# Kernel tuning notes

Measured on AMD Instinct MI355X. Metric: run time of the kernel, lower is better.

## Reference

```python
import jax, jax.numpy as jnp
import numpy as np
import math

BS, C, H, W, D = 2, 64, 32, 16, 32
FLAT = H * W * D          # 16384 voxels
N = 2048                  # non-empty voxels per sample (fixed for jit)
K = 256                   # min(int(0.2 * N), max_k=256)
EPS = 1e-5


def _pe(c, length):
    # sinusoidal positional encoding, interleaved sin/cos as in the torch code
    pos = jnp.arange(length, dtype=jnp.float32)[:, None]
    div = jnp.exp(jnp.arange(0, c, 2, dtype=jnp.float32) * (-math.log(10000.0) / c))
    ang = pos * div[None, :]                     # [length, c//2]
    return jnp.stack([jnp.sin(ang), jnp.cos(ang)], axis=-1).reshape(length, c)


def _bn(z, g, b):
    # eval-mode BatchNorm1d with running_mean=0, running_var=1
    return z * (g / jnp.sqrt(1.0 + EPS)) + b


def setup_inputs() -> dict:
    key = jax.random.key(0)
    ks = jax.random.split(key, 8)
    rng = np.random.default_rng(0)
    mask_idx = np.stack([np.sort(rng.choice(FLAT, size=N, replace=False)) for _ in range(BS)])
    w = lambda k, s: jax.random.normal(k, s, jnp.float32) * 0.05
    return dict(
        input=jax.random.normal(ks[0], (BS, C, H, W, D), jnp.float32),
        mask_idx=jnp.asarray(mask_idx, jnp.int32),
        w_ne1=w(ks[1], (C, 32)), b_ne1=jnp.zeros(32), g_ne=jnp.ones(32), be_ne=jnp.zeros(32),
        w_ne2=w(ks[2], (32, 1)), b_ne2=jnp.zeros(1),
        w_p1=w(ks[3], (C, 32)), b_p1=jnp.zeros(32), g_p1=jnp.ones(32), be_p1=jnp.zeros(32),
        w_p2=w(ks[4], (32, 32)), b_p2=jnp.zeros(32), g_p2=jnp.ones(32), be_p2=jnp.zeros(32),
        w_p3=w(ks[5], (32, 1)), b_p3=jnp.zeros(1),
        w_r1=w(ks[6], (4 * C, 2 * C)), b_r1=jnp.zeros(2 * C),
        w_r2=w(ks[7], (2 * C, C)), b_r2=jnp.zeros(C),
    )


def reference(input, mask_idx, w_ne1, b_ne1, g_ne, be_ne, w_ne2, b_ne2,
              w_p1, b_p1, g_p1, be_p1, w_p2, b_p2, g_p2, be_p2, w_p3, b_p3,
              w_r1, b_r1, w_r2, b_r2):
    bs, c = input.shape[0], input.shape[1]
    pe = _pe(c, FLAT)
    x = input                         # agg (external Bottleneck3D stack) ~ identity
    x_flat = x.reshape(bs, c, FLAT)

    def per_sample(xf, idx, key):
        mpe = pe[idx]                                  # [N, c] masked positional enc
        xi = xf[:, idx].T + mpe                        # [N, c] masked gather
        h1 = jax.nn.relu(_bn(xi @ w_ne1 + b_ne1, g_ne, be_ne))
        prob = jax.nn.sigmoid((h1 @ w_ne2 + b_ne2)[:, 0])    # [N] non-empty prob
        # torch.multinomial(prob, K, replacement=True)
        topk = jax.random.categorical(key, jnp.log(prob), shape=(K,))
        tf = xi[topk]                                  # [K, c] sampled features
        ne_k = prob[topk]                              # [K]
        # xi_repeat + tiled masked_pe[topk]  ->  [N, K, c]
        xw = xi[:, None, :] + mpe[topk][None, :, :]
        hp = jax.nn.relu(_bn(xw @ w_p1 + b_p1, g_p1, be_p1))
        hp = jax.nn.relu(_bn(hp @ w_p2 + b_p2, g_p2, be_p2))
        P = jax.nn.sigmoid((hp @ w_p3 + b_p3)[..., 0])  # [N, K]
        Pi = P * ne_k[None, :]
        Pe_ = (1.0 - P) * ne_k[None, :]
        x_intra = (Pi @ tf) / jnp.sum(Pi, axis=1, keepdims=True)   # [N, c]
        x_inter = (Pe_ @ tf) / jnp.sum(Pe_, axis=1, keepdims=True)
        ctx = jnp.zeros((2 * c, FLAT), input.dtype)
        ctx = ctx.at[:c, idx].set(x_intra.T).at[c:, idx].set(x_inter.T)
        return ctx

    keys = jax.random.split(jax.random.key(42), bs)
    ctx = jax.vmap(per_sample)(x_flat, mask_idx, keys).reshape(bs, 2 * c, H, W, D)
    xcat = jnp.concatenate([input, ctx, x], axis=1)     # [bs, 4c, H, W, D]
    # resize: the two defined 1x1 Conv3d layers (Bottleneck3D blocks are external)
    y = jnp.einsum('bchwd,cf->bfhwd', xcat, w_r1) + b_r1[None, :, None, None, None]
    y = jnp.einsum('bchwd,cf->bfhwd', y, w_r2) + b_r2[None, :, None, None, None]
    return y
```

## Files before the change

### kernel.cpp

```cpp
#include <hip/hip_runtime.h>
#include <cstdint>
#include <cmath>

#define BS    2
#define CC    64
#define FLAT  16384
#define NN    2048
#define KK    256
#define EPSBN 1e-5f
#define TINYF 1.17549435e-38f
#define PE_SCALE -0.14391156831212787f
#define JAX_PARTITIONABLE 1

#define OFF_XI    0
#define OFF_XI1   (OFF_XI   + BS*NN*CC)
#define OFF_PROB  (OFF_XI1  + BS*NN*32)
#define OFF_LOGP  (OFF_PROB + BS*NN)
#define OFF_NEK   (OFF_LOGP + BS*NN)
#define OFF_TF    (OFF_NEK  + BS*KK)
#define OFF_M1    (OFF_TF   + BS*KK*CC)
#define OFF_DELTA (OFF_M1   + BS*KK*32)
#define OFF_WF    (OFF_DELTA+ BS*NN*CC)
#define OFF_BF    (OFF_WF   + 256*CC)
#define OFF_INV   (OFF_BF   + CC)

__device__ __forceinline__ uint32_t rotl32(uint32_t x, int r) {
  return (x << r) | (x >> (32 - r));
}
__device__ __forceinline__ void tf2x32(uint32_t k0, uint32_t k1,
                                       uint32_t& x0, uint32_t& x1) {
  uint32_t k2 = k0 ^ k1 ^ 0x1BD11BDAu;
  x0 += k0; x1 += k1;
#define TFR(r) { x0 += x1; x1 = rotl32(x1, r); x1 ^= x0; }
  TFR(13) TFR(15) TFR(26) TFR(6)  x0 += k1; x1 += k2 + 1u;
  TFR(17) TFR(29) TFR(16) TFR(24) x0 += k2; x1 += k0 + 2u;
  TFR(13) TFR(15) TFR(26) TFR(6)  x0 += k0; x1 += k1 + 3u;
  TFR(17) TFR(29) TFR(16) TFR(24) x0 += k1; x1 += k2 + 4u;
  TFR(13) TFR(15) TFR(26) TFR(6)  x0 += k2; x1 += k0 + 5u;
#undef TFR
}
__device__ __forceinline__ void jax_key(int b, uint32_t& k0, uint32_t& k1) {
#if JAX_PARTITIONABLE
  uint32_t x0 = 0u, x1 = (uint32_t)b;
  tf2x32(0u, 42u, x0, x1);
  k0 = x0; k1 = x1;
#else
  uint32_t a0 = 0u, a1 = 2u, c0 = 1u, c1 = 3u;
  tf2x32(0u, 42u, a0, a1);
  tf2x32(0u, 42u, c0, c1);
  if (b == 0) { k0 = a0; k1 = c0; } else { k0 = a1; k1 = c1; }
#endif
}
__device__ __forceinline__ uint32_t jax_bits(uint32_t k0, uint32_t k1, uint32_t i) {
#if JAX_PARTITIONABLE
  uint32_t x0 = 0u, x1 = i;
  tf2x32(k0, k1, x0, x1);
  return x0 ^ x1;
#else
  const uint32_t half = (uint32_t)(KK * NN) / 2u;
  uint32_t x0, x1;
  if (i < half) { x0 = i; x1 = i + half; tf2x32(k0, k1, x0, x1); return x0; }
  else          { x0 = i - half; x1 = i; tf2x32(k0, k1, x0, x1); return x1; }
#endif
}

__global__ void k0_fold(const float* __restrict__ w_r1, const float* __restrict__ b_r1,
                        const float* __restrict__ w_r2, const float* __restrict__ b_r2,
                        float* __restrict__ ws) {
  int c = blockIdx.x;
  int co = threadIdx.x;
  float acc = 0.f;
  for (int f = 0; f < 128; ++f)
    acc += w_r1[c * 128 + f] * w_r2[f * 64 + co];
  ws[OFF_WF + c * 64 + co] = acc;
  if (blockIdx.x == 0) {
    float bb = b_r2[co];
    for (int f = 0; f < 128; ++f) bb += b_r1[f] * w_r2[f * 64 + co];
    ws[OFF_BF + co] = bb;
  }
  int* inv = (int*)(ws + OFF_INV);
  int t = blockIdx.x * 64 + threadIdx.x;
  inv[t] = -1;
  inv[t + BS * FLAT / 2] = -1;
}

__global__ __launch_bounds__(256) void k1_xi(
    const float* __restrict__ input, const int* __restrict__ midx,
    const float* __restrict__ w_ne1, const float* __restrict__ b_ne1,
    const float* __restrict__ g_ne,  const float* __restrict__ be_ne,
    const float* __restrict__ w_ne2, const float* __restrict__ b_ne2,
    const float* __restrict__ w_p1,  const float* __restrict__ g_p1,
    float* __restrict__ ws) {
  int tid = threadIdx.x;
  int j = tid & 31, nl = tid >> 5;
  int bn = blockIdx.x * 8 + nl;
  int b = bn >> 11, n = bn & (NN - 1);
  int pos = midx[b * NN + n];
  __shared__ float xis[8][66];
  float d = expf((float)(2 * j) * PE_SCALE);
  float ang = (float)pos * d;
  float xs = sinf(ang) + input[((size_t)(b * CC + 2 * j)) * FLAT + pos];
  float xc = cosf(ang) + input[((size_t)(b * CC + 2 * j + 1)) * FLAT + pos];
  xis[nl][2 * j] = xs; xis[nl][2 * j + 1] = xc;
  float2 v2; v2.x = xs; v2.y = xc;
  ((float2*)(ws + OFF_XI + (size_t)(b * NN + n) * CC))[j] = v2;
  __syncthreads();
  float zne = b_ne1[j];
  float z1 = 0.f;
#pragma unroll
  for (int c2 = 0; c2 < CC; ++c2) {
    float xv = xis[nl][c2];
    zne += xv * w_ne1[c2 * 32 + j];
    z1  += xv * w_p1[c2 * 32 + j];
  }
  float ane = g_ne[j] / sqrtf(1.f + EPSBN);
  float h = fmaxf(0.f, zne * ane + be_ne[j]);
  float pp = h * w_ne2[j];
  for (int off = 16; off > 0; off >>= 1) pp += __shfl_down(pp, off, 32);
  if (j == 0) {
    float prob = 1.f / (1.f + expf(-(pp + b_ne2[0])));
    ws[OFF_PROB + b * NN + n] = prob;
    ws[OFF_LOGP + b * NN + n] = logf(prob);
    ((int*)(ws + OFF_INV))[b * FLAT + pos] = n;
  }
  float a1 = g_p1[j] / sqrtf(1.f + EPSBN);
  ws[OFF_XI1 + (size_t)(b * NN + n) * 32 + j] = z1 * a1;
}

__global__ __launch_bounds__(256) void k2_sample(
    const int* __restrict__ midx,
    const float* __restrict__ w_p1, const float* __restrict__ b_p1,
    const float* __restrict__ g_p1, const float* __restrict__ be_p1,
    float* __restrict__ ws) {
  int b = blockIdx.x >> 8, k = blockIdx.x & 255;
  int tid = threadIdx.x;
  uint32_t kb0, kb1;
  jax_key(b, kb0, kb1);
  const float* logp = ws + OFF_LOGP + b * NN;
  const float NEGINF = -__builtin_inff();
  float bv = NEGINF; int bn = NN;
#pragma unroll 1
  for (int r = 0; r < 8; ++r) {
    int n = r * 256 + tid;
    uint32_t bits = jax_bits(kb0, kb1, (uint32_t)(k * NN + n));
    float f = __uint_as_float(0x3f800000u | (bits >> 9)) - 1.0f;
    float u = fmaxf(TINYF, f + TINYF);
    float gmb = -logf(-logf(u));
    float v = logp[n] + gmb;
    if (v > bv || (v == bv && n < bn)) { bv = v; bn = n; }
  }
  __shared__ float sv[256];
  __shared__ int   sn[256];
  __shared__ float mpe[CC];
  sv[tid] = bv; sn[tid] = bn;
  __syncthreads();
  for (int s = 128; s > 0; s >>= 1) {
    if (tid < s) {
      float v2 = sv[tid + s]; int n2 = sn[tid + s];
      if (v2 > sv[tid] || (v2 == sv[tid] && n2 < sn[tid])) { sv[tid] = v2; sn[tid] = n2; }
    }
    __syncthreads();
  }
  int best = sn[0];
  if (tid == 0)
    ws[OFF_NEK + b * KK + k] = ws[OFF_PROB + b * NN + best];
  if (tid < CC) {
    int c = tid;
    ws[OFF_TF + (size_t)(b * KK + k) * CC + c] =
        ws[OFF_XI + (size_t)(b * NN + best) * CC + c];
    int pos = midx[b * NN + best];
    int jj = c >> 1;
    float ang = (float)pos * expf((float)(2 * jj) * PE_SCALE);
    mpe[c] = (c & 1) ? cosf(ang) : sinf(ang);
  }
  __syncthreads();
  if (tid < 32) {
    int jj = tid;
    float acc = b_p1[jj];
#pragma unroll
    for (int c = 0; c < CC; ++c) acc += mpe[c] * w_p1[c * 32 + jj];
    float a = g_p1[jj] / sqrtf(1.f + EPSBN);
    ws[OFF_M1 + (size_t)(b * KK + k) * 32 + jj] = acc * a + be_p1[jj];
  }
}

__global__ __launch_bounds__(256) void k3_fused(
    const float* __restrict__ w_p2, const float* __restrict__ b_p2,
    const float* __restrict__ g_p2, const float* __restrict__ be_p2,
    const float* __restrict__ w_p3, const float* __restrict__ b_p3,
    float* __restrict__ ws) {
  __shared__ __align__(16) float m1t[32 * 132];
  __shared__ __align__(16) float w2s[1024];
  __shared__ __align__(16) float Pis[4][256];
  __shared__ __align__(16) float nekl[256];
  __shared__ __align__(16) float xi1s[4][32];
  __shared__ __align__(16) float c2f[32];
  __shared__ __align__(16) float w3l[32];
  __shared__ float sI[4], sE[4];
  int tid = threadIdx.x;
  int b = blockIdx.x >> 9;
  int n0 = (blockIdx.x & 511) * 4;
  int nn  = tid >> 6;
  int kgl = (tid >> 2) & 15;
  int qg  = tid & 3;
  int k0l = kgl * 8, q0 = qg * 8;
  for (int e = tid; e < 1024; e += 256) {
    int q = e & 31;
    w2s[e] = w_p2[e] * (g_p2[q] / sqrtf(1.f + EPSBN));
  }
  if (tid < 32) {
    c2f[tid] = b_p2[tid] * (g_p2[tid] / sqrtf(1.f + EPSBN)) + be_p2[tid];
    w3l[tid] = w_p3[tid];
  }
  if (tid < 128) {
    int n4 = tid >> 5, jx = tid & 31;
    xi1s[n4][jx] = ws[OFF_XI1 + (size_t)(b * NN + n0 + n4) * 32 + jx];
  }
  nekl[tid] = ws[OFF_NEK + b * KK + tid];
  float b3 = b_p3[0];
  __syncthreads();
  float4 cva = *(const float4*)&c2f[q0];
  float4 cvb = *(const float4*)&c2f[q0 + 4];
  float4 w3a = *(const float4*)&w3l[q0];
  float4 w3b = *(const float4*)&w3l[q0 + 4];
#pragma unroll 1
  for (int kh = 0; kh < 2; ++kh) {
    for (int e = tid; e < 1024; e += 256) {
      int kl = e >> 3, q = e & 7;
      float4 v = *(const float4*)(ws + OFF_M1 +
                   (size_t)(b * KK + kh * 128 + kl) * 32 + q * 4);
      m1t[(q * 4 + 0) * 132 + kl] = v.x;
      m1t[(q * 4 + 1) * 132 + kl] = v.y;
      m1t[(q * 4 + 2) * 132 + kl] = v.z;
      m1t[(q * 4 + 3) * 132 + kl] = v.w;
    }
    __syncthreads();
    float z[8][8];
#pragma unroll
    for (int i = 0; i < 8; ++i) {
      z[i][0] = cva.x; z[i][1] = cva.y; z[i][2] = cva.z; z[i][3] = cva.w;
      z[i][4] = cvb.x; z[i][5] = cvb.y; z[i][6] = cvb.z; z[i][7] = cvb.w;
    }
#pragma unroll 4
    for (int jj = 0; jj < 32; ++jj) {
      float xv = xi1s[nn][jj];
      const float4* mr = (const float4*)&m1t[jj * 132 + k0l];
      float4 ma = mr[0], mb = mr[1];
      const float4* wr = (const float4*)&w2s[jj * 32 + q0];
      float4 wa = wr[0], wb = wr[1];
      float h0 = fmaxf(0.f, xv + ma.x), h1 = fmaxf(0.f, xv + ma.y);
      float h2 = fmaxf(0.f, xv + ma.z), h3 = fmaxf(0.f, xv + ma.w);
      float h4 = fmaxf(0.f, xv + mb.x), h5 = fmaxf(0.f, xv + mb.y);
      float h6 = fmaxf(0.f, xv + mb.z), h7 = fmaxf(0.f, xv + mb.w);
#define ZROW(i, hh) \
      z[i][0] += hh * wa.x; z[i][1] += hh * wa.y; z[i][2] += hh * wa.z; z[i][3] += hh * wa.w; \
      z[i][4] += hh * wb.x; z[i][5] += hh * wb.y; z[i][6] += hh * wb.z; z[i][7] += hh * wb.w;
      ZROW(0, h0) ZROW(1, h1) ZROW(2, h2) ZROW(3, h3)
      ZROW(4, h4) ZROW(5, h5) ZROW(6, h6) ZROW(7, h7)
#undef ZROW
    }
    float s[8];
#pragma unroll
    for (int i = 0; i < 8; ++i)
      s[i] = fmaxf(0.f, z[i][0]) * w3a.x + fmaxf(0.f, z[i][1]) * w3a.y
           + fmaxf(0.f, z[i][2]) * w3a.z + fmaxf(0.f, z[i][3]) * w3a.w
           + fmaxf(0.f, z[i][4]) * w3b.x + fmaxf(0.f, z[i][5]) * w3b.y
           + fmaxf(0.f, z[i][6]) * w3b.z + fmaxf(0.f, z[i][7]) * w3b.w;
#pragma unroll
    for (int i = 0; i < 8; ++i) {
      s[i] += __shfl_xor(s[i], 1, 64);
      s[i] += __shfl_xor(s[i], 2, 64);
    }
    float sv0 = qg < 2 ? (qg == 0 ? s[0] : s[1]) : (qg == 2 ? s[2] : s[3]);
    float sv1 = qg < 2 ? (qg == 0 ? s[4] : s[5]) : (qg == 2 ? s[6] : s[7]);
    int kg0 = kh * 128 + k0l;
    float P0 = 1.f / (1.f + expf(-(sv0 + b3)));
    float P1 = 1.f / (1.f + expf(-(sv1 + b3)));
    Pis[nn][kg0 + qg]     = P0 * nekl[kg0 + qg];
    Pis[nn][kg0 + 4 + qg] = P1 * nekl[kg0 + 4 + qg];
    __syncthreads();
  }
  float* xIl = m1t;
  float* xEl = m1t + 272;
  if (tid < 128) {
    int n4 = tid >> 5, jx = tid & 31;
    float s1 = 0.f, s2 = 0.f;
#pragma unroll
    for (int t = 0; t < 8; ++t) {
      float pi = Pis[n4][jx + 32 * t];
      s1 += pi;
      s2 += nekl[jx + 32 * t] - pi;
    }
    for (int off = 16; off > 0; off >>= 1) {
      s1 += __shfl_down(s1, off, 32);
      s2 += __shfl_down(s2, off, 32);
    }
    if (jx == 0) { sI[n4] = s1; sE[n4] = s2; }
  }
  __syncthreads();
  {
    int c = tid & 63, n = tid >> 6;
    const float4* PI4 = (const float4*)Pis[n];
    const float4* NE4 = (const float4*)nekl;
    const float* tfg = ws + OFF_TF + (size_t)b * KK * CC + c;
    float aI = 0.f, aE = 0.f;
#pragma unroll 4
    for (int kq = 0; kq < 64; ++kq) {
      float4 piv = PI4[kq], nev = NE4[kq];
      float t0 = tfg[(4 * kq + 0) * 64];
      float t1 = tfg[(4 * kq + 1) * 64];
      float t2 = tfg[(4 * kq + 2) * 64];
      float t3 = tfg[(4 * kq + 3) * 64];
      aI += piv.x * t0 + piv.y * t1 + piv.z * t2 + piv.w * t3;
      aE += (nev.x - piv.x) * t0 + (nev.y - piv.y) * t1
          + (nev.z - piv.z) * t2 + (nev.w - piv.w) * t3;
    }
    xIl[n * 68 + c] = aI / sI[n];
    xEl[n * 68 + c] = aE / sE[n];
  }
  __syncthreads();
  {
    int co = tid & 63, n4 = tid >> 6;
    const float4* xI4 = (const float4*)&xIl[n4 * 68];
    const float4* xE4 = (const float4*)&xEl[n4 * 68];
    const float* wI = ws + OFF_WF + 64 * CC + co;
    const float* wE = ws + OFF_WF + 128 * CC + co;
    float dsum = 0.f;
#pragma unroll 4
    for (int cq = 0; cq < 16; ++cq) {
      float4 xi4 = xI4[cq], xe4 = xE4[cq];
      dsum += xi4.x * wI[(4 * cq + 0) * 64] + xi4.y * wI[(4 * cq + 1) * 64]
            + xi4.z * wI[(4 * cq + 2) * 64] + xi4.w * wI[(4 * cq + 3) * 64];
      dsum += xe4.x * wE[(4 * cq + 0) * 64] + xe4.y * wE[(4 * cq + 1) * 64]
            + xe4.z * wE[(4 * cq + 2) * 64] + xe4.w * wE[(4 * cq + 3) * 64];
    }
    ws[OFF_DELTA + (size_t)(b * NN + n0 + n4) * CC + co] = dsum;
  }
}

__global__ __launch_bounds__(256) void k4_out(
    const float* __restrict__ input, float* __restrict__ out,
    const float* __restrict__ ws) {
  __shared__ __align__(16) float wfa[64 * 64];
  __shared__ float bfl[64];
  int tid = threadIdx.x;
  const float* wf = ws + OFF_WF;
  for (int e = tid; e < 4096; e += 256) {
    int c = e >> 6, co = e & 63;
    wfa[e] = wf[c * 64 + co] + wf[(192 + c) * 64 + co];
  }
  if (tid < 64) bfl[tid] = ws[OFF_BF + tid];
  __syncthreads();
  int q = tid >> 6, lane = tid & 63;
  int pg = blockIdx.x * 64 + lane;
  int b = pg >> 14, pos = pg & (FLAT - 1);
  const int* inv = (const int*)(ws + OFF_INV);
  float acc[16];
#pragma unroll
  for (int u = 0; u < 16; ++u) acc[u] = bfl[q * 16 + u];
#pragma unroll 4
  for (int c = 0; c < 64; ++c) {
    float xv = input[((size_t)(b * CC + c)) * FLAT + pos];
    const float4* wr = (const float4*)&wfa[c * 64 + q * 16];
#pragma unroll
    for (int u4 = 0; u4 < 4; ++u4) {
      float4 w = wr[u4];
      acc[u4 * 4 + 0] += xv * w.x; acc[u4 * 4 + 1] += xv * w.y;
      acc[u4 * 4 + 2] += xv * w.z; acc[u4 * 4 + 3] += xv * w.w;
    }
  }
  int n = inv[pg];
  if (n >= 0) {
    const float4* dr = (const float4*)(ws + OFF_DELTA + (size_t)(b * NN + n) * CC + q * 16);
#pragma unroll
    for (int u4 = 0; u4 < 4; ++u4) {
      float4 dv = dr[u4];
      acc[u4 * 4 + 0] += dv.x; acc[u4 * 4 + 1] += dv.y;
      acc[u4 * 4 + 2] += dv.z; acc[u4 * 4 + 3] += dv.w;
    }
  }
#pragma unroll
  for (int u = 0; u < 16; ++u)
    out[((size_t)(b * CC + q * 16 + u)) * FLAT + pos] = acc[u];
}

extern "C" void kernel_launch(void* const* d_in, const int* in_sizes, int n_in,
                              void* d_out, int out_size, void* d_ws, size_t ws_size,
                              hipStream_t stream) {
  const float* input = (const float*)d_in[0];
  const int*   midx  = (const int*)  d_in[1];
  const float* w_ne1 = (const float*)d_in[2];
  const float* b_ne1 = (const float*)d_in[3];
  const float* g_ne  = (const float*)d_in[4];
  const float* be_ne = (const float*)d_in[5];
  const float* w_ne2 = (const float*)d_in[6];
  const float* b_ne2 = (const float*)d_in[7];
  const float* w_p1  = (const float*)d_in[8];
  const float* b_p1  = (const float*)d_in[9];
  const float* g_p1  = (const float*)d_in[10];
  const float* be_p1 = (const float*)d_in[11];
  const float* w_p2  = (const float*)d_in[12];
  const float* b_p2  = (const float*)d_in[13];
  const float* g_p2  = (const float*)d_in[14];
  const float* be_p2 = (const float*)d_in[15];
  const float* w_p3  = (const float*)d_in[16];
  const float* b_p3  = (const float*)d_in[17];
  const float* w_r1  = (const float*)d_in[18];
  const float* b_r1  = (const float*)d_in[19];
  const float* w_r2  = (const float*)d_in[20];
  const float* b_r2  = (const float*)d_in[21];
  float* out = (float*)d_out;
  float* ws  = (float*)d_ws;

  k0_fold<<<dim3(256), dim3(64), 0, stream>>>(w_r1, b_r1, w_r2, b_r2, ws);
  k1_xi<<<dim3(BS * NN / 8), dim3(256), 0, stream>>>(
      input, midx, w_ne1, b_ne1, g_ne, be_ne, w_ne2, b_ne2, w_p1, g_p1, ws);
  k2_sample<<<dim3(BS * KK), dim3(256), 0, stream>>>(
      midx, w_p1, b_p1, g_p1, be_p1, ws);
  k3_fused<<<dim3(BS * NN / 4), dim3(256), 0, stream>>>(
      w_p2, b_p2, g_p2, be_p2, w_p3, b_p3, ws);
  k4_out<<<dim3(BS * FLAT / 64), dim3(256), 0, stream>>>(input, out, ws);
}
```

Measured before the change: 182.1 us.

## Shrink per-thread register tiles in k3 and split k4 output channels across blocks

In k3, each thread now accumulates an 8x4 tile instead of 8x8 and loops over two k-halves, and the M1 transpose load uses unpadded rows with a different thread mapping. xIl/xEl get their own shared arrays instead of aliasing m1t. In k4, each block now computes only 16 of the 64 output channels, giving four times as many blocks with smaller weight tiles and fewer accumulators. The aim is lower register pressure and higher occupancy, at the cost of re-reading the input four times in k4 and possible LDS bank conflicts from removing the padding.

```diff
diff --git a/kernel.cpp b/kernel.cpp
--- a/kernel.cpp
+++ b/kernel.cpp
@@ -189,21 +189,22 @@
     const float* __restrict__ g_p2, const float* __restrict__ be_p2,
     const float* __restrict__ w_p3, const float* __restrict__ b_p3,
     float* __restrict__ ws) {
-  __shared__ __align__(16) float m1t[32 * 132];
+  __shared__ __align__(16) float m1t[32 * 128];
   __shared__ __align__(16) float w2s[1024];
   __shared__ __align__(16) float Pis[4][256];
   __shared__ __align__(16) float nekl[256];
   __shared__ __align__(16) float xi1s[4][32];
   __shared__ __align__(16) float c2f[32];
   __shared__ __align__(16) float w3l[32];
+  __shared__ __align__(16) float xIl[4 * 68], xEl[4 * 68];
   __shared__ float sI[4], sE[4];
   int tid = threadIdx.x;
   int b = blockIdx.x >> 9;
   int n0 = (blockIdx.x & 511) * 4;
-  int nn  = tid >> 6;
-  int kgl = (tid >> 2) & 15;
-  int qg  = tid & 3;
-  int k0l = kgl * 8, q0 = qg * 8;
+  int nn = tid >> 6;
+  int kg = (tid >> 3) & 7;
+  int qg = tid & 7;
+  int q0 = qg * 4;
   for (int e = tid; e < 1024; e += 256) {
     int q = e & 31;
     w2s[e] = w_p2[e] * (g_p2[q] / sqrtf(1.f + EPSBN));
@@ -219,69 +220,69 @@
   nekl[tid] = ws[OFF_NEK + b * KK + tid];
   float b3 = b_p3[0];
   __syncthreads();
-  float4 cva = *(const float4*)&c2f[q0];
-  float4 cvb = *(const float4*)&c2f[q0 + 4];
-  float4 w3a = *(const float4*)&w3l[q0];
-  float4 w3b = *(const float4*)&w3l[q0 + 4];
+  const float4* w2s4 = (const float4*)w2s;
+  const float4 cv  = *(const float4*)&c2f[q0];
+  const float4 w3v = *(const float4*)&w3l[q0];
 #pragma unroll 1
   for (int kh = 0; kh < 2; ++kh) {
-    for (int e = tid; e < 1024; e += 256) {
-      int kl = e >> 3, q = e & 7;
-      float4 v = *(const float4*)(ws + OFF_M1 +
-                   (size_t)(b * KK + kh * 128 + kl) * 32 + q * 4);
-      m1t[(q * 4 + 0) * 132 + kl] = v.x;
-      m1t[(q * 4 + 1) * 132 + kl] = v.y;
-      m1t[(q * 4 + 2) * 132 + kl] = v.z;
-      m1t[(q * 4 + 3) * 132 + kl] = v.w;
+    {
+      int kl = tid & 127, jh = tid >> 7;
+      const float4* src = (const float4*)(ws + OFF_M1 +
+                           (size_t)(b * KK + kh * 128 + kl) * 32 + jh * 16);
+#pragma unroll
+      for (int u = 0; u < 4; ++u) {
+        float4 v = src[u];
+        m1t[(jh * 16 + u * 4 + 0) * 128 + kl] = v.x;
+        m1t[(jh * 16 + u * 4 + 1) * 128 + kl] = v.y;
+        m1t[(jh * 16 + u * 4 + 2) * 128 + kl] = v.z;
+        m1t[(jh * 16 + u * 4 + 3) * 128 + kl] = v.w;
+      }
     }
     __syncthreads();
-    float z[8][8];
-#pragma unroll
-    for (int i = 0; i < 8; ++i) {
-      z[i][0] = cva.x; z[i][1] = cva.y; z[i][2] = cva.z; z[i][3] = cva.w;
-      z[i][4] = cvb.x; z[i][5] = cvb.y; z[i][6] = cvb.z; z[i][7] = cvb.w;
-    }
-#pragma unroll 4
-    for (int jj = 0; jj < 32; ++jj) {
-      float xv = xi1s[nn][jj];
-      const float4* mr = (const float4*)&m1t[jj * 132 + k0l];
-      float4 ma = mr[0], mb = mr[1];
-      const float4* wr = (const float4*)&w2s[jj * 32 + q0];
-      float4 wa = wr[0], wb = wr[1];
-      float h0 = fmaxf(0.f, xv + ma.x), h1 = fmaxf(0.f, xv + ma.y);
-      float h2 = fmaxf(0.f, xv + ma.z), h3 = fmaxf(0.f, xv + ma.w);
-      float h4 = fmaxf(0.f, xv + mb.x), h5 = fmaxf(0.f, xv + mb.y);
-      float h6 = fmaxf(0.f, xv + mb.z), h7 = fmaxf(0.f, xv + mb.w);
+#pragma unroll 1
+    for (int kp = 0; kp < 2; ++kp) {
+      int k0l = kp * 64 + kg * 8;
+      float z[8][4];
+#pragma unroll
+      for (int i = 0; i < 8; ++i) {
+        z[i][0] = cv.x; z[i][1] = cv.y; z[i][2] = cv.z; z[i][3] = cv.w;
+      }
+#pragma unroll 8
+      for (int jj = 0; jj < 32; ++jj) {
+        float xv = xi1s[nn][jj];
+        const float4* mr = (const float4*)&m1t[jj * 128 + k0l];
+        float4 ma = mr[0], mb = mr[1];
+        const float4 w = w2s4[jj * 8 + qg];
+        float h0 = fmaxf(0.f, xv + ma.x), h1 = fmaxf(0.f, xv + ma.y);
+        float h2 = fmaxf(0.f, xv + ma.z), h3 = fmaxf(0.f, xv + ma.w);
+        float h4 = fmaxf(0.f, xv + mb.x), h5 = fmaxf(0.f, xv + mb.y);
+        float h6 = fmaxf(0.f, xv + mb.z), h7 = fmaxf(0.f, xv + mb.w);
 #define ZROW(i, hh) \
-      z[i][0] += hh * wa.x; z[i][1] += hh * wa.y; z[i][2] += hh * wa.z; z[i][3] += hh * wa.w; \
-      z[i][4] += hh * wb.x; z[i][5] += hh * wb.y; z[i][6] += hh * wb.z; z[i][7] += hh * wb.w;
-      ZROW(0, h0) ZROW(1, h1) ZROW(2, h2) ZROW(3, h3)
-      ZROW(4, h4) ZROW(5, h5) ZROW(6, h6) ZROW(7, h7)
+        z[i][0] += hh * w.x; z[i][1] += hh * w.y; \
+        z[i][2] += hh * w.z; z[i][3] += hh * w.w;
+        ZROW(0, h0) ZROW(1, h1) ZROW(2, h2) ZROW(3, h3)
+        ZROW(4, h4) ZROW(5, h5) ZROW(6, h6) ZROW(7, h7)
 #undef ZROW
-    }
-    float s[8];
-#pragma unroll
-    for (int i = 0; i < 8; ++i)
-      s[i] = fmaxf(0.f, z[i][0]) * w3a.x + fmaxf(0.f, z[i][1]) * w3a.y
-           + fmaxf(0.f, z[i][2]) * w3a.z + fmaxf(0.f, z[i][3]) * w3a.w
-           + fmaxf(0.f, z[i][4]) * w3b.x + fmaxf(0.f, z[i][5]) * w3b.y
-           + fmaxf(0.f, z[i][6]) * w3b.z + fmaxf(0.f, z[i][7]) * w3b.w;
-#pragma unroll
-    for (int i = 0; i < 8; ++i) {
-      s[i] += __shfl_xor(s[i], 1, 64);
-      s[i] += __shfl_xor(s[i], 2, 64);
-    }
-    float sv0 = qg < 2 ? (qg == 0 ? s[0] : s[1]) : (qg == 2 ? s[2] : s[3]);
-    float sv1 = qg < 2 ? (qg == 0 ? s[4] : s[5]) : (qg == 2 ? s[6] : s[7]);
-    int kg0 = kh * 128 + k0l;
-    float P0 = 1.f / (1.f + expf(-(sv0 + b3)));
-    float P1 = 1.f / (1.f + expf(-(sv1 + b3)));
-    Pis[nn][kg0 + qg]     = P0 * nekl[kg0 + qg];
-    Pis[nn][kg0 + 4 + qg] = P1 * nekl[kg0 + 4 + qg];
+      }
+      float s[8];
+#pragma unroll
+      for (int i = 0; i < 8; ++i)
+        s[i] = fmaxf(0.f, z[i][0]) * w3v.x + fmaxf(0.f, z[i][1]) * w3v.y
+             + fmaxf(0.f, z[i][2]) * w3v.z + fmaxf(0.f, z[i][3]) * w3v.w;
+#pragma unroll
+      for (int i = 0; i < 8; ++i) {
+        s[i] += __shfl_xor(s[i], 1, 64);
+        s[i] += __shfl_xor(s[i], 2, 64);
+        s[i] += __shfl_xor(s[i], 4, 64);
+      }
+      float sv = qg < 4 ? (qg < 2 ? (qg == 0 ? s[0] : s[1]) : (qg == 2 ? s[2] : s[3]))
+                        : (qg < 6 ? (qg == 4 ? s[4] : s[5]) : (qg == 6 ? s[6] : s[7]));
+      int kown = kh * 128 + k0l + qg;
+      float P = 1.f / (1.f + expf(-(sv + b3)));
+      Pis[nn][kown] = P * nekl[kown];
+    }
     __syncthreads();
   }
-  float* xIl = m1t;
-  float* xEl = m1t + 272;
   if (tid < 128) {
     int n4 = tid >> 5, jx = tid & 31;
     float s1 = 0.f, s2 = 0.f;
@@ -341,47 +342,40 @@
 __global__ __launch_bounds__(256) void k4_out(
     const float* __restrict__ input, float* __restrict__ out,
     const float* __restrict__ ws) {
-  __shared__ __align__(16) float wfa[64 * 64];
-  __shared__ float bfl[64];
+  __shared__ __align__(16) float wfa[64 * 16];
+  __shared__ float bfl[16];
   int tid = threadIdx.x;
+  int cq = blockIdx.x & 3, pgrp = blockIdx.x >> 2;
   const float* wf = ws + OFF_WF;
-  for (int e = tid; e < 4096; e += 256) {
-    int c = e >> 6, co = e & 63;
-    wfa[e] = wf[c * 64 + co] + wf[(192 + c) * 64 + co];
-  }
-  if (tid < 64) bfl[tid] = ws[OFF_BF + tid];
+  for (int e = tid; e < 1024; e += 256) {
+    int c = e >> 4, i = e & 15;
+    wfa[e] = wf[c * 64 + cq * 16 + i] + wf[(192 + c) * 64 + cq * 16 + i];
+  }
+  if (tid < 16) bfl[tid] = ws[OFF_BF + cq * 16 + tid];
   __syncthreads();
   int q = tid >> 6, lane = tid & 63;
-  int pg = blockIdx.x * 64 + lane;
+  int pg = pgrp * 64 + lane;
   int b = pg >> 14, pos = pg & (FLAT - 1);
   const int* inv = (const int*)(ws + OFF_INV);
-  float acc[16];
-#pragma unroll
-  for (int u = 0; u < 16; ++u) acc[u] = bfl[q * 16 + u];
+  float acc[4];
+#pragma unroll
+  for (int u = 0; u < 4; ++u) acc[u] = bfl[q * 4 + u];
 #pragma unroll 4
   for (int c = 0; c < 64; ++c) {
     float xv = input[((size_t)(b * CC + c)) * FLAT + pos];
-    const float4* wr = (const float4*)&wfa[c * 64 + q * 16];
-#pragma unroll
-    for (int u4 = 0; u4 < 4; ++u4) {
-      float4 w = wr[u4];
-      acc[u4 * 4 + 0] += xv * w.x; acc[u4 * 4 + 1] += xv * w.y;
-      acc[u4 * 4 + 2] += xv * w.z; acc[u4 * 4 + 3] += xv * w.w;
-    }
+    float4 w = *(const float4*)&wfa[c * 16 + q * 4];
+    acc[0] += xv * w.x; acc[1] += xv * w.y;
+    acc[2] += xv * w.z; acc[3] += xv * w.w;
   }
   int n = inv[pg];
   if (n >= 0) {
-    const float4* dr = (const float4*)(ws + OFF_DELTA + (size_t)(b * NN + n) * CC + q * 16);
-#pragma unroll
-    for (int u4 = 0; u4 < 4; ++u4) {
-      float4 dv = dr[u4];
-      acc[u4 * 4 + 0] += dv.x; acc[u4 * 4 + 1] += dv.y;
-      acc[u4 * 4 + 2] += dv.z; acc[u4 * 4 + 3] += dv.w;
-    }
-  }
-#pragma unroll
-  for (int u = 0; u < 16; ++u)
-    out[((size_t)(b * CC + q * 16 + u)) * FLAT + pos] = acc[u];
+    float4 dv = *(const float4*)(ws + OFF_DELTA +
+                  (size_t)(b * NN + n) * CC + cq * 16 + q * 4);
+    acc[0] += dv.x; acc[1] += dv.y; acc[2] += dv.z; acc[3] += dv.w;
+  }
+#pragma unroll
+  for (int u = 0; u < 4; ++u)
+    out[((size_t)(b * CC + cq * 16 + q * 4 + u)) * FLAT + pos] = acc[u];
 }
 
 extern "C" void kernel_launch(void* const* d_in, const int* in_sizes, int n_in,
@@ -419,5 +413,5 @@
       midx, w_p1, b_p1, g_p1, be_p1, ws);
   k3_fused<<<dim3(BS * NN / 4), dim3(256), 0, stream>>>(
       w_p2, b_p2, g_p2, be_p2, w_p3, b_p3, ws);
-  k4_out<<<dim3(BS * FLAT / 64), dim3(256), 0, stream>>>(input, out, ws);
-}
+  k4_out<<<dim3(BS * FLAT / 64 * 4), dim3(256), 0, stream>>>(input, out, ws);
+}
```

Result: no change. 184.6 us (+1.4%).
